# Kernel optimization log

Hardware: AMD Instinct MI355X
Metric: run time of the kernel (lower is better)

The kernel has to match this reference:

```python
import jax, jax.numpy as jnp
import numpy as np
import math

DIM = 1024
NUM_HEADS = 16
SHARED_HEADS = 1
ROUTED_HEADS = 3
HEAD_DIM = DIM // NUM_HEADS
B, N = 2, 2048


def setup_inputs() -> dict:
    key = jax.random.key(0)
    ks = jax.random.split(key, 16)
    s = 1.0 / math.sqrt(DIM)
    inp = {
        "x": jax.random.normal(ks[0], (B, N, DIM), dtype=jnp.float32),
        "Wq": jax.random.uniform(ks[1], (DIM, DIM), minval=-s, maxval=s),
        "bq": jax.random.uniform(ks[2], (DIM,), minval=-s, maxval=s),
        "Wk": jax.random.uniform(ks[3], (DIM, DIM), minval=-s, maxval=s),
        "bk": jax.random.uniform(ks[4], (DIM,), minval=-s, maxval=s),
        "Wv": jax.random.uniform(ks[5], (DIM, DIM), minval=-s, maxval=s),
        "bv": jax.random.uniform(ks[6], (DIM,), minval=-s, maxval=s),
        "Wp": jax.random.uniform(ks[7], (DIM, DIM), minval=-s, maxval=s),
        "bp": jax.random.uniform(ks[8], (DIM,), minval=-s, maxval=s),
        "Wr": jax.random.uniform(ks[9], (NUM_HEADS - SHARED_HEADS, DIM), minval=-s, maxval=s),
        "br": jax.random.uniform(ks[10], (NUM_HEADS - SHARED_HEADS,), minval=-s, maxval=s),
        "Ws": jax.random.uniform(ks[11], (2, DIM), minval=-s, maxval=s),
        "bs": jax.random.uniform(ks[12], (2,), minval=-s, maxval=s),
        # temperature init: log(exp(1/0.24)-1), shape (H,1,1)
        "temperature": jnp.full((NUM_HEADS, 1, 1), float(np.log(np.expm1(1.0 / 0.24))), dtype=jnp.float32),
        "query_embedding": 0.02 * jax.random.normal(ks[13], (NUM_HEADS, 1, HEAD_DIM), dtype=jnp.float32),
    }
    return inp


def reference(x, Wq, bq, Wk, bk, Wv, bv, Wp, bp, Wr, br, Ws, bs, temperature, query_embedding):
    Bsz, Nn, C = x.shape
    H, hd = NUM_HEADS, HEAD_DIM

    def heads(W, b):
        y = x @ W.T + b  # [B,N,C]
        return y.reshape(Bsz, Nn, H, hd).transpose(0, 2, 1, 3)  # [B,H,N,hd]

    q = heads(Wq, bq)
    k = heads(Wk, bk)
    v = heads(Wv, bv)

    q_norm = q / jnp.linalg.norm(q, axis=-1, keepdims=True)
    q_scaled = (q_norm + query_embedding[None]) * jax.nn.softplus(temperature)[None]
    attn = jnp.einsum("bhqd,bhkd->bhqk", q_scaled, k) / math.sqrt(hd)
    attn = jax.nn.softmax(attn, axis=-1)
    h = jnp.einsum("bhqk,bhkd->bhqd", attn, v)
    h = h.transpose(0, 2, 1, 3).reshape(Bsz, Nn, C)  # [B,N,C]

    # routed-head gating
    gates = jax.nn.softmax(h @ Wr.T + br, axis=-1)  # [B,N,H-shared]
    _, idx = jax.lax.top_k(gates, ROUTED_HEADS)
    # NOTE: original uses num_classes=num_heads-shared_heads for one_hot
    mask = jax.nn.one_hot(idx, H - SHARED_HEADS, dtype=gates.dtype).sum(axis=-2)
    routed_gates = gates * mask * ROUTED_HEADS

    sw = jax.nn.softmax(h @ Ws.T + bs, axis=-1)  # [B,N,2]
    shared_gates = sw * SHARED_HEADS
    weight_0 = sw * 2.0
    shared_gates = weight_0[..., 0:1] * shared_gates
    routed_gates = weight_0[..., 1:2] * routed_gates
    masked_gates = jnp.concatenate([shared_gates, routed_gates], axis=-1)

    # einsum('bnc,bnd->bnd') == per-token scalar sum over c times h
    out = h * masked_gates.sum(axis=-1, keepdims=True)
    return out @ Wp.T + bp
```

## Files before the change

### kernel.cpp

```cpp
#include <hip/hip_runtime.h>
#include <hip/hip_bf16.h>

typedef short s16x8 __attribute__((ext_vector_type(8)));
typedef float f32x4 __attribute__((ext_vector_type(4)));
typedef float f32x16 __attribute__((ext_vector_type(16)));

__device__ __forceinline__ float b2f(unsigned short u) {
    union { unsigned int i; float f; } v;
    v.i = ((unsigned int)u) << 16;
    return v.f;
}
__device__ __forceinline__ unsigned int pkbf16(float a, float b) {
    union { __hip_bfloat162 h; unsigned int u; } v;
    v.h = __float22bfloat162_rn(make_float2(a, b));
    return v.u;
}
__device__ __forceinline__ float fast_exp2(float x) {
#if __has_builtin(__builtin_amdgcn_exp2f)
    return __builtin_amdgcn_exp2f(x);
#else
    return exp2f(x);
#endif
}

__device__ __forceinline__ void gl_lds16(const unsigned short* g, unsigned short* l) {
    __builtin_amdgcn_global_load_lds(
        (const __attribute__((address_space(1))) void*)g,
        (__attribute__((address_space(3))) void*)l, 16, 0, 0);
}

__device__ __forceinline__ void perm32swap(unsigned int &a, unsigned int &b) {
    asm("v_permlane32_swap_b32 %0, %1" : "+v"(a), "+v"(b));
}

__device__ __forceinline__ s16x8 mk8(unsigned int a, unsigned int b,
                                     unsigned int c, unsigned int d) {
    union { uint4 u; s16x8 h; } v;
    v.u = make_uint4(a, b, c, d);
    return v.h;
}

__device__ __forceinline__ void cvt8(const float* __restrict__ s,
                                     unsigned short* __restrict__ d, int i) {
    const float* p = s + (size_t)i * 8;
    float4 a = *(const float4*)p;
    float4 b = *(const float4*)(p + 4);
    unsigned int u0 = pkbf16(a.x, a.y), u1 = pkbf16(a.z, a.w);
    unsigned int u2 = pkbf16(b.x, b.y), u3 = pkbf16(b.z, b.w);
    uint4 o = {u0, u1, u2, u3};
    *(uint4*)&d[(size_t)i * 8] = o;
}

__global__ __launch_bounds__(256) void cvt_main(
    const float* __restrict__ x,  const float* __restrict__ Wq,
    const float* __restrict__ Wk, const float* __restrict__ Wv,
    const float* __restrict__ Wr, const float* __restrict__ Ws,
    const float* __restrict__ bq, const float* __restrict__ bk,
    const float* __restrict__ bv,
    unsigned short* __restrict__ xb, unsigned short* __restrict__ wqkv,
    unsigned short* __restrict__ wg, float* __restrict__ bqkv)
{
    int blk = blockIdx.x, t = threadIdx.x;
    if (blk < 2048)      cvt8(x,  xb,             blk * 256 + t);
    else if (blk < 2560) cvt8(Wq, wqkv,           (blk - 2048) * 256 + t);
    else if (blk < 3072) cvt8(Wk, wqkv + 1048576, (blk - 2560) * 256 + t);
    else if (blk < 3584) cvt8(Wv, wqkv + 2097152, (blk - 3072) * 256 + t);
    else if (blk < 3592) { int i = (blk - 3584) * 256 + t; if (i < 1920) cvt8(Wr, wg, i); }
    else if (blk < 3593) { int i = t; cvt8(Ws, wg + 15360, i); }
    else {
        int i = (blk - 3593) * 256 + t;
        bqkv[i] = (i < 1024) ? bq[i] : (i < 2048) ? bk[i - 1024] : bv[i - 2048];
    }
}

__global__ __launch_bounds__(256) void qkv_gemm(
    const unsigned short* __restrict__ A,
    const unsigned short* __restrict__ Bw,
    const float* __restrict__ bias,
    unsigned short* __restrict__ Q, unsigned short* __restrict__ K,
    unsigned short* __restrict__ Vt)
{
    __shared__ __attribute__((aligned(16))) unsigned short As[128 * 64];
    __shared__ __attribute__((aligned(16))) unsigned short Bs[128 * 64];
    const int t = threadIdx.x;
    const int wave = t >> 6, lane = t & 63;
    const int m0 = blockIdx.x * 128, n0 = blockIdx.y * 128;
    const int wm = (wave >> 1) * 64, wn = (wave & 1) * 64;
    const int lr = lane & 15, lq = lane >> 4;
    const int srow = lane >> 3;
    const int scol = (((lane & 7) ^ srow) << 3);

    f32x4 acc[4][4];
#pragma unroll
    for (int i = 0; i < 4; ++i)
#pragma unroll
        for (int j = 0; j < 4; ++j) acc[i][j] = (f32x4){0.f, 0.f, 0.f, 0.f};

    for (int k0 = 0; k0 < 1024; k0 += 64) {
        __syncthreads();
#pragma unroll
        for (int i = 0; i < 4; ++i) {
            int rb = wave * 32 + i * 8;
            gl_lds16(&A[(size_t)(m0 + rb + srow) * 1024 + k0 + scol], &As[rb * 64]);
            gl_lds16(&Bw[(size_t)(n0 + rb + srow) * 1024 + k0 + scol], &Bs[rb * 64]);
        }
        __syncthreads();
#pragma unroll
        for (int kk = 0; kk < 64; kk += 32) {
            const int po = ((((kk >> 3) + lq) ^ (lr & 7)) << 3);
            s16x8 af[4], bf[4];
#pragma unroll
            for (int i = 0; i < 4; ++i)
                af[i] = *(const s16x8*)&As[(wm + i * 16 + lr) * 64 + po];
#pragma unroll
            for (int j = 0; j < 4; ++j)
                bf[j] = *(const s16x8*)&Bs[(wn + j * 16 + lr) * 64 + po];
#pragma unroll
            for (int i = 0; i < 4; ++i)
#pragma unroll
                for (int j = 0; j < 4; ++j)
                    acc[i][j] = __builtin_amdgcn_mfma_f32_16x16x32_bf16(af[i], bf[j], acc[i][j], 0, 0, 0);
        }
    }
    const int kind = n0 >> 10;
    const int nc = n0 & 1023;
    if (kind < 2) {
        unsigned short* Cm = kind ? K : Q;
#pragma unroll
        for (int j = 0; j < 4; ++j) {
            int cl = wn + j * 16 + lr;
            float bv = bias[n0 + cl];
#pragma unroll
            for (int i = 0; i < 4; ++i) {
                int rowb = m0 + wm + i * 16 + lq * 4;
                unsigned int u0 = pkbf16(acc[i][j][0] + bv, acc[i][j][1] + bv);
                unsigned int u1 = pkbf16(acc[i][j][2] + bv, acc[i][j][3] + bv);
                Cm[(size_t)(rowb + 0) * 1024 + nc + cl] = (unsigned short)u0;
                Cm[(size_t)(rowb + 1) * 1024 + nc + cl] = (unsigned short)(u0 >> 16);
                Cm[(size_t)(rowb + 2) * 1024 + nc + cl] = (unsigned short)u1;
                Cm[(size_t)(rowb + 3) * 1024 + nc + cl] = (unsigned short)(u1 >> 16);
            }
        }
    } else {
        const int bb = m0 >> 11;
#pragma unroll
        for (int j = 0; j < 4; ++j) {
            int col = nc + wn + j * 16 + lr;
            int hh = col >> 6, dd = col & 63;
            float bv = bias[n0 + wn + j * 16 + lr];
#pragma unroll
            for (int i = 0; i < 4; ++i) {
                int tokb = m0 + wm + i * 16 + lq * 4;
                int tloc = tokb & 2047;
                uint2 u;
                u.x = pkbf16(acc[i][j][0] + bv, acc[i][j][1] + bv);
                u.y = pkbf16(acc[i][j][2] + bv, acc[i][j][3] + bv);
                *(uint2*)&Vt[((size_t)(bb * 16 + hh) * 64 + dd) * 2048 + tloc] = u;
            }
        }
    }
}

__global__ __launch_bounds__(256) void attn_kernel(
    const unsigned short* __restrict__ Q,
    const unsigned short* __restrict__ Kb,
    const unsigned short* __restrict__ Vt,
    const float* __restrict__ temp,
    const float* __restrict__ qe,
    unsigned short* __restrict__ Hout)
{
    __shared__ __attribute__((aligned(16))) unsigned short Ks[2][64 * 64];
    __shared__ __attribute__((aligned(16))) unsigned short Vs[2][64 * 64];
    __shared__ float Lred[4][32];
    const int t = threadIdx.x, wave = t >> 6, lane = t & 63;
    const int l31 = lane & 31, hi = lane >> 5;
    const int bh = blockIdx.x, b = bh >> 4, h = bh & 15;
    const int q0 = blockIdx.y * 128;
    const int srow = lane >> 3;
    const int scol = (((lane & 7) ^ srow) << 3);
    unsigned short* KsF = &Ks[0][0];

    auto stageK = [&](int kc, int cb) {
#pragma unroll
        for (int i2 = 0; i2 < 2; ++i2) {
            int rb = wave * 16 + i2 * 8;
            gl_lds16(&Kb[(size_t)(b * 2048 + kc + rb + srow) * 1024 + h * 64 + scol],
                     &Ks[cb][rb * 64]);
        }
    };
    auto stageV = [&](int kc, int cb) {
#pragma unroll
        for (int i2 = 0; i2 < 2; ++i2) {
            int rb = wave * 16 + i2 * 8;
            gl_lds16(&Vt[((size_t)(b * 16 + h) * 64 + rb + srow) * 2048 + kc + scol],
                     &Vs[cb][rb * 64]);
        }
    };

#pragma unroll
    for (int i = 0; i < 4; ++i) {
        int rb = wave * 32 + i * 8;
        gl_lds16(&Q[(size_t)(b * 2048 + q0 + rb + srow) * 1024 + h * 64 + scol],
                 &KsF[rb * 64]);
    }
    __syncthreads();

    s16x8 qf[4];
#pragma unroll
    for (int kd = 0; kd < 4; ++kd)
        qf[kd] = *(const s16x8*)&KsF[(wave * 32 + l31) * 64 + (((kd * 2 + hi) ^ (l31 & 7)) << 3)];
    __syncthreads();

    stageK(0, 0);
    stageV(0, 0);

    float tv = temp[h];
    float sp = ((tv > 20.f) ? tv : log1pf(__expf(tv))) * 0.18033688f;
    s16x8 aqB[4];
    {
        float v[4][8];
        float ss = 0.f;
#pragma unroll
        for (int kd = 0; kd < 4; ++kd)
#pragma unroll
            for (int e = 0; e < 8; ++e) {
                v[kd][e] = b2f((unsigned short)qf[kd][e]);
                ss += v[kd][e] * v[kd][e];
            }
        ss += __shfl_xor(ss, 32);
        float rn = rsqrtf(ss);
#pragma unroll
        for (int kd = 0; kd < 4; ++kd) {
            const float* qh = qe + h * 64 + kd * 16 + hi * 8;
            unsigned int w0 = pkbf16((v[kd][0] * rn + qh[0]) * sp, (v[kd][1] * rn + qh[1]) * sp);
            unsigned int w1 = pkbf16((v[kd][2] * rn + qh[2]) * sp, (v[kd][3] * rn + qh[3]) * sp);
            unsigned int w2 = pkbf16((v[kd][4] * rn + qh[4]) * sp, (v[kd][5] * rn + qh[5]) * sp);
            unsigned int w3 = pkbf16((v[kd][6] * rn + qh[6]) * sp, (v[kd][7] * rn + qh[7]) * sp);
            aqB[kd] = mk8(w0, w1, w2, w3);
        }
    }

    f32x16 accO[2];
#pragma unroll
    for (int r = 0; r < 16; ++r) { accO[0][r] = 0.f; accO[1][r] = 0.f; }
    float lsum = 0.f;

    for (int it = 0; it < 32; ++it) {
        const int c = it & 1;
        __syncthreads();
        if (it < 31) { stageK((it + 1) * 64, c ^ 1); stageV((it + 1) * 64, c ^ 1); }

#pragma unroll
        for (int jj = 0; jj < 2; ++jj) {
            const int j = jj ^ (wave & 1);

            s16x8 kf[4];
#pragma unroll
            for (int kd = 0; kd < 4; ++kd)
                kf[kd] = *(const s16x8*)&Ks[c][(j * 32 + l31) * 64 + (((kd * 2 + hi) ^ (l31 & 7)) << 3)];
            f32x16 s;
#pragma unroll
            for (int r = 0; r < 16; ++r) s[r] = 0.f;
            __builtin_amdgcn_s_setprio(1);
#pragma unroll
            for (int kd = 0; kd < 4; ++kd)
                s = __builtin_amdgcn_mfma_f32_32x32x16_bf16(kf[kd], aqB[kd], s, 0, 0, 0);
            __builtin_amdgcn_s_setprio(0);

            float p[16];
#pragma unroll
            for (int r = 0; r < 16; ++r) p[r] = fast_exp2(s[r]);
            lsum += (((p[0] + p[1]) + (p[2] + p[3])) + ((p[4] + p[5]) + (p[6] + p[7])))
                  + (((p[8] + p[9]) + (p[10] + p[11])) + ((p[12] + p[13]) + (p[14] + p[15])));
            unsigned int u[8];
#pragma unroll
            for (int g = 0; g < 8; ++g) u[g] = pkbf16(p[2 * g], p[2 * g + 1]);

#pragma unroll
            for (int kh = 0; kh < 2; ++kh) {
                unsigned int a0 = u[4 * kh + 0], b0 = u[4 * kh + 2];
                unsigned int a1 = u[4 * kh + 1], b1 = u[4 * kh + 3];
                perm32swap(a0, b0);
                perm32swap(a1, b1);
                s16x8 pf = mk8(a0, a1, b0, b1);
                const int vb = (((j * 4 + kh * 2 + hi) ^ (l31 & 7)) << 3);
                s16x8 v0 = *(const s16x8*)&Vs[c][(l31) * 64 + vb];
                s16x8 v1 = *(const s16x8*)&Vs[c][(32 + l31) * 64 + vb];
                __builtin_amdgcn_s_setprio(1);
                accO[0] = __builtin_amdgcn_mfma_f32_32x32x16_bf16(pf, v0, accO[0], 0, 0, 0);
                accO[1] = __builtin_amdgcn_mfma_f32_32x32x16_bf16(pf, v1, accO[1], 0, 0, 0);
                __builtin_amdgcn_s_setprio(0);
            }
        }
    }

    lsum += __shfl_xor(lsum, 32);
    if (hi == 0) Lred[wave][l31] = 1.f / lsum;
    __syncthreads();
    float invv[16];
#pragma unroll
    for (int r = 0; r < 16; ++r)
        invv[r] = Lred[wave][(r & 3) + 8 * (r >> 2) + 4 * hi];
#pragma unroll
    for (int jd = 0; jd < 2; ++jd)
#pragma unroll
        for (int r = 0; r < 16; ++r) {
            int qrow = (r & 3) + 8 * (r >> 2) + 4 * hi;
            float val = accO[jd][r] * invv[r];
            Hout[(size_t)(b * 2048 + q0 + wave * 32 + qrow) * 1024 + h * 64 + jd * 32 + l31] =
                (unsigned short)pkbf16(val, val);
        }
}

__global__ __launch_bounds__(256) void gate_g(
    const unsigned short* __restrict__ Hb,
    const unsigned short* __restrict__ Wg,
    const float* __restrict__ br, const float* __restrict__ bs,
    const float* __restrict__ Wp, unsigned short* __restrict__ wpb,
    float* __restrict__ g)
{
    __shared__ __attribute__((aligned(16))) unsigned short As[4][16 * 64];
    __shared__ __attribute__((aligned(16))) unsigned short Gs[4][32 * 64];
    __shared__ float Lred[4][16][32];
    const int t = threadIdx.x, wave = t >> 6, lane = t & 63;
    const int lr = lane & 15, lq = lane >> 4;
    const int m0 = blockIdx.x * 16;
    const int srow = lane >> 3;
    const int scol = (((lane & 7) ^ srow) << 3);

    cvt8(Wp, wpb, blockIdx.x * 512 + t);
    cvt8(Wp, wpb, blockIdx.x * 512 + 256 + t);

    f32x4 acc[2];
    acc[0] = (f32x4){0.f, 0.f, 0.f, 0.f};
    acc[1] = (f32x4){0.f, 0.f, 0.f, 0.f};

    for (int k0 = wave * 64; k0 < 1024; k0 += 256) {
        gl_lds16(&Hb[(size_t)(m0 + srow) * 1024 + k0 + scol], &As[wave][0]);
        gl_lds16(&Hb[(size_t)(m0 + 8 + srow) * 1024 + k0 + scol], &As[wave][8 * 64]);
#pragma unroll
        for (int i = 0; i < 4; ++i) {
            int row = i * 8 + srow;
            int wr = (row > 16) ? 16 : row;
            gl_lds16(&Wg[(size_t)wr * 1024 + k0 + scol], &Gs[wave][i * 8 * 64]);
        }
        __syncthreads();
#pragma unroll
        for (int kk = 0; kk < 64; kk += 32) {
            const int po = ((((kk >> 3) + lq) ^ (lr & 7)) << 3);
            s16x8 af = *(const s16x8*)&As[wave][lr * 64 + po];
#pragma unroll
            for (int j = 0; j < 2; ++j) {
                s16x8 gf = *(const s16x8*)&Gs[wave][(j * 16 + lr) * 64 + po];
                acc[j] = __builtin_amdgcn_mfma_f32_16x16x32_bf16(af, gf, acc[j], 0, 0, 0);
            }
        }
    }
#pragma unroll
    for (int j = 0; j < 2; ++j)
#pragma unroll
        for (int r = 0; r < 4; ++r)
            Lred[wave][lq * 4 + r][j * 16 + lr] = acc[j][r];
    __syncthreads();
    if (t < 16) {
        float lg[17];
#pragma unroll
        for (int j = 0; j < 17; ++j)
            lg[j] = Lred[0][t][j] + Lred[1][t][j] + Lred[2][t][j] + Lred[3][t][j]
                  + ((j < 15) ? br[j] : bs[j - 15]);
        float mx = lg[0];
#pragma unroll
        for (int j = 1; j < 15; ++j) mx = fmaxf(mx, lg[j]);
        float sum = 0.f, v1 = -1.f, v2 = -1.f, v3 = -1.f;
#pragma unroll
        for (int j = 0; j < 15; ++j) {
            float e = __expf(lg[j] - mx);
            sum += e;
            if (e > v1)      { v3 = v2; v2 = v1; v1 = e; }
            else if (e > v2) { v3 = v2; v2 = e; }
            else if (e > v3) { v3 = e; }
        }
        float tops = (v1 + v2 + v3) / sum;
        float sm = fmaxf(lg[15], lg[16]);
        float e0 = __expf(lg[15] - sm), e1 = __expf(lg[16] - sm);
        float inv = 1.f / (e0 + e1);
        g[m0 + t] = 2.f * (e0 * inv) + 6.f * (e1 * inv) * tops;
    }
}

__global__ __launch_bounds__(256) void gemm64_out(
    const unsigned short* __restrict__ A,
    const unsigned short* __restrict__ Bw,
    const float* __restrict__ bias,
    const float* __restrict__ g,
    float* __restrict__ C)
{
    __shared__ __attribute__((aligned(16))) unsigned short As[64 * 64];
    __shared__ __attribute__((aligned(16))) unsigned short Bs[64 * 64];
    const int t = threadIdx.x, wave = t >> 6, lane = t & 63;
    const int lr = lane & 15, lq = lane >> 4;
    const int m0 = blockIdx.x * 64, n0 = blockIdx.y * 64;
    const int wm = (wave >> 1) * 32, wn = (wave & 1) * 32;
    const int srow = lane >> 3;
    const int scol = (((lane & 7) ^ srow) << 3);

    f32x4 acc[2][2];
#pragma unroll
    for (int i = 0; i < 2; ++i)
#pragma unroll
        for (int j = 0; j < 2; ++j) acc[i][j] = (f32x4){0.f, 0.f, 0.f, 0.f};

    for (int k0 = 0; k0 < 1024; k0 += 64) {
        __syncthreads();
#pragma unroll
        for (int i = 0; i < 2; ++i) {
            int rb = wave * 16 + i * 8;
            gl_lds16(&A[(size_t)(m0 + rb + srow) * 1024 + k0 + scol], &As[rb * 64]);
            gl_lds16(&Bw[(size_t)(n0 + rb + srow) * 1024 + k0 + scol], &Bs[rb * 64]);
        }
        __syncthreads();
#pragma unroll
        for (int kk = 0; kk < 64; kk += 32) {
            const int po = ((((kk >> 3) + lq) ^ (lr & 7)) << 3);
            s16x8 af[2], bf[2];
#pragma unroll
            for (int i = 0; i < 2; ++i)
                af[i] = *(const s16x8*)&As[(wm + i * 16 + lr) * 64 + po];
#pragma unroll
            for (int j = 0; j < 2; ++j)
                bf[j] = *(const s16x8*)&Bs[(wn + j * 16 + lr) * 64 + po];
#pragma unroll
            for (int i = 0; i < 2; ++i)
#pragma unroll
                for (int j = 0; j < 2; ++j)
                    acc[i][j] = __builtin_amdgcn_mfma_f32_16x16x32_bf16(af[i], bf[j], acc[i][j], 0, 0, 0);
        }
    }
#pragma unroll
    for (int i = 0; i < 2; ++i) {
        const float4 gi = *(const float4*)&g[m0 + wm + i * 16 + lq * 4];
        float gv[4] = {gi.x, gi.y, gi.z, gi.w};
#pragma unroll
        for (int j = 0; j < 2; ++j) {
            int col = n0 + wn + j * 16 + lr;
            float bv = bias[col];
            int rowb = m0 + wm + i * 16 + lq * 4;
#pragma unroll
            for (int r = 0; r < 4; ++r)
                C[(size_t)(rowb + r) * 1024 + col] = acc[i][j][r] * gv[r] + bv;
        }
    }
}

extern "C" void kernel_launch(void* const* d_in, const int* in_sizes, int n_in,
                              void* d_out, int out_size, void* d_ws, size_t ws_size,
                              hipStream_t stream)
{
    (void)in_sizes; (void)n_in; (void)out_size; (void)ws_size;
    const float* x   = (const float*)d_in[0];
    const float* Wq  = (const float*)d_in[1];
    const float* bq  = (const float*)d_in[2];
    const float* Wk  = (const float*)d_in[3];
    const float* bk  = (const float*)d_in[4];
    const float* Wv  = (const float*)d_in[5];
    const float* bv  = (const float*)d_in[6];
    const float* Wp  = (const float*)d_in[7];
    const float* bp  = (const float*)d_in[8];
    const float* Wr  = (const float*)d_in[9];
    const float* br  = (const float*)d_in[10];
    const float* Ws  = (const float*)d_in[11];
    const float* bs  = (const float*)d_in[12];
    const float* temperature = (const float*)d_in[13];
    const float* qe  = (const float*)d_in[14];
    float* out = (float*)d_out;

    const size_t MB = 1048576;
    unsigned short* qb   = (unsigned short*)d_ws;
    unsigned short* kb   = (unsigned short*)((char*)d_ws + 8 * MB);
    unsigned short* hb   = (unsigned short*)((char*)d_ws + 16 * MB);
    unsigned short* wqkv = (unsigned short*)((char*)d_ws + 24 * MB);
    unsigned short* wg   = (unsigned short*)((char*)d_ws + 30 * MB);
    float*          bqkv = (float*)((char*)d_ws + 30 * MB + 65536);
    float*          gbuf = (float*)((char*)d_ws + 30 * MB + 131072);
    unsigned short* xb = (unsigned short*)d_out;
    unsigned short* vt = xb + 4 * MB;
    unsigned short* wpb = qb;

    dim3 blk(256);
    cvt_main<<<dim3(3605), blk, 0, stream>>>(x, Wq, Wk, Wv, Wr, Ws, bq, bk, bv,
                                             xb, wqkv, wg, bqkv);
    qkv_gemm<<<dim3(32, 24), blk, 0, stream>>>(xb, wqkv, bqkv, qb, kb, vt);
    attn_kernel<<<dim3(32, 16), blk, 0, stream>>>(qb, kb, vt, temperature, qe, hb);
    gate_g<<<dim3(256), blk, 0, stream>>>(hb, wg, br, bs, Wp, wpb, gbuf);
    gemm64_out<<<dim3(64, 16), blk, 0, stream>>>(hb, wpb, bp, gbuf, out);
}
```

Baseline: 215.8 us.

## Split attention key range across two wave groups per block and merge partials

Attention blocks now run 8 waves: two groups of four each process half of the key sequence for the same 128 queries, using separate double-buffered K/V LDS tiles. After the loop, the second group writes its partial output accumulators to LDS and the first group adds them and divides by the combined row sums. This halves the serial key loop per wave and raises resident waves per CU, at the cost of doubled LDS per block and an extra reduction and barrier at the end.

Measured after the change: 212.5 us. No clear change (-1.5%).

```diff
diff --git a/kernel.cpp b/kernel.cpp
--- a/kernel.cpp
+++ b/kernel.cpp
@@ -161,7 +161,7 @@
     }
 }
 
-__global__ __launch_bounds__(256) void attn_kernel(
+__global__ __launch_bounds__(512, 4) void attn_kernel(
     const unsigned short* __restrict__ Q,
     const unsigned short* __restrict__ Kb,
     const unsigned short* __restrict__ Vt,
@@ -169,46 +169,49 @@
     const float* __restrict__ qe,
     unsigned short* __restrict__ Hout)
 {
-    __shared__ __attribute__((aligned(16))) unsigned short Ks[2][64 * 64];
-    __shared__ __attribute__((aligned(16))) unsigned short Vs[2][64 * 64];
-    __shared__ float Lred[4][32];
+    __shared__ __attribute__((aligned(16))) unsigned short Ks[2][2][64 * 64];
+    __shared__ __attribute__((aligned(16))) unsigned short Vs[2][2][64 * 64];
+    __shared__ float Lred[8][32];
     const int t = threadIdx.x, wave = t >> 6, lane = t & 63;
+    const int ws = wave >> 2, wq = wave & 3;
     const int l31 = lane & 31, hi = lane >> 5;
     const int bh = blockIdx.x, b = bh >> 4, h = bh & 15;
     const int q0 = blockIdx.y * 128;
     const int srow = lane >> 3;
     const int scol = (((lane & 7) ^ srow) << 3);
-    unsigned short* KsF = &Ks[0][0];
+    const int kbase = ws << 10;
+    unsigned short* KsF = &Ks[0][0][0];
 
     auto stageK = [&](int kc, int cb) {
 #pragma unroll
         for (int i2 = 0; i2 < 2; ++i2) {
-            int rb = wave * 16 + i2 * 8;
-            gl_lds16(&Kb[(size_t)(b * 2048 + kc + rb + srow) * 1024 + h * 64 + scol],
-                     &Ks[cb][rb * 64]);
+            int rb = wq * 16 + i2 * 8;
+            gl_lds16(&Kb[(size_t)(b * 2048 + kbase + kc + rb + srow) * 1024 + h * 64 + scol],
+                     &Ks[ws][cb][rb * 64]);
         }
     };
     auto stageV = [&](int kc, int cb) {
 #pragma unroll
         for (int i2 = 0; i2 < 2; ++i2) {
-            int rb = wave * 16 + i2 * 8;
-            gl_lds16(&Vt[((size_t)(b * 16 + h) * 64 + rb + srow) * 2048 + kc + scol],
-                     &Vs[cb][rb * 64]);
+            int rb = wq * 16 + i2 * 8;
+            gl_lds16(&Vt[((size_t)(b * 16 + h) * 64 + rb + srow) * 2048 + kbase + kc + scol],
+                     &Vs[ws][cb][rb * 64]);
         }
     };
 
-#pragma unroll
-    for (int i = 0; i < 4; ++i) {
-        int rb = wave * 32 + i * 8;
+    {
+        int rb = wave * 16;
         gl_lds16(&Q[(size_t)(b * 2048 + q0 + rb + srow) * 1024 + h * 64 + scol],
                  &KsF[rb * 64]);
+        gl_lds16(&Q[(size_t)(b * 2048 + q0 + rb + 8 + srow) * 1024 + h * 64 + scol],
+                 &KsF[(rb + 8) * 64]);
     }
     __syncthreads();
 
     s16x8 qf[4];
 #pragma unroll
     for (int kd = 0; kd < 4; ++kd)
-        qf[kd] = *(const s16x8*)&KsF[(wave * 32 + l31) * 64 + (((kd * 2 + hi) ^ (l31 & 7)) << 3)];
+        qf[kd] = *(const s16x8*)&KsF[(wq * 32 + l31) * 64 + (((kd * 2 + hi) ^ (l31 & 7)) << 3)];
     __syncthreads();
 
     stageK(0, 0);
@@ -245,10 +248,10 @@
     for (int r = 0; r < 16; ++r) { accO[0][r] = 0.f; accO[1][r] = 0.f; }
     float lsum = 0.f;
 
-    for (int it = 0; it < 32; ++it) {
+    for (int it = 0; it < 16; ++it) {
         const int c = it & 1;
         __syncthreads();
-        if (it < 31) { stageK((it + 1) * 64, c ^ 1); stageV((it + 1) * 64, c ^ 1); }
+        if (it < 15) { stageK((it + 1) * 64, c ^ 1); stageV((it + 1) * 64, c ^ 1); }
 
 #pragma unroll
         for (int jj = 0; jj < 2; ++jj) {
@@ -257,7 +260,7 @@
             s16x8 kf[4];
 #pragma unroll
             for (int kd = 0; kd < 4; ++kd)
-                kf[kd] = *(const s16x8*)&Ks[c][(j * 32 + l31) * 64 + (((kd * 2 + hi) ^ (l31 & 7)) << 3)];
+                kf[kd] = *(const s16x8*)&Ks[ws][c][(j * 32 + l31) * 64 + (((kd * 2 + hi) ^ (l31 & 7)) << 3)];
             f32x16 s;
 #pragma unroll
             for (int r = 0; r < 16; ++r) s[r] = 0.f;
@@ -284,8 +287,8 @@
                 perm32swap(a1, b1);
                 s16x8 pf = mk8(a0, a1, b0, b1);
                 const int vb = (((j * 4 + kh * 2 + hi) ^ (l31 & 7)) << 3);
-                s16x8 v0 = *(const s16x8*)&Vs[c][(l31) * 64 + vb];
-                s16x8 v1 = *(const s16x8*)&Vs[c][(32 + l31) * 64 + vb];
+                s16x8 v0 = *(const s16x8*)&Vs[ws][c][(l31) * 64 + vb];
+                s16x8 v1 = *(const s16x8*)&Vs[ws][c][(32 + l31) * 64 + vb];
                 __builtin_amdgcn_s_setprio(1);
                 accO[0] = __builtin_amdgcn_mfma_f32_32x32x16_bf16(pf, v0, accO[0], 0, 0, 0);
                 accO[1] = __builtin_amdgcn_mfma_f32_32x32x16_bf16(pf, v1, accO[1], 0, 0, 0);
@@ -295,21 +298,43 @@
     }
 
     lsum += __shfl_xor(lsum, 32);
-    if (hi == 0) Lred[wave][l31] = 1.f / lsum;
+    if (hi == 0) Lred[wave][l31] = lsum;
     __syncthreads();
-    float invv[16];
-#pragma unroll
-    for (int r = 0; r < 16; ++r)
-        invv[r] = Lred[wave][(r & 3) + 8 * (r >> 2) + 4 * hi];
-#pragma unroll
-    for (int jd = 0; jd < 2; ++jd)
-#pragma unroll
-        for (int r = 0; r < 16; ++r) {
-            int qrow = (r & 3) + 8 * (r >> 2) + 4 * hi;
-            float val = accO[jd][r] * invv[r];
-            Hout[(size_t)(b * 2048 + q0 + wave * 32 + qrow) * 1024 + h * 64 + jd * 32 + l31] =
-                (unsigned short)pkbf16(val, val);
-        }
+
+    float* mb = (wq < 2) ? (float*)&Ks[0][wq][0] : (float*)&Vs[0][wq - 2][0];
+    if (ws == 1) {
+#pragma unroll
+        for (int jd = 0; jd < 2; ++jd)
+#pragma unroll
+            for (int rg = 0; rg < 4; ++rg) {
+                f32x4 vv = { accO[jd][rg * 4 + 0], accO[jd][rg * 4 + 1],
+                             accO[jd][rg * 4 + 2], accO[jd][rg * 4 + 3] };
+                *(f32x4*)&mb[((jd * 4 + rg) << 8) + (lane << 2)] = vv;
+            }
+    }
+    __syncthreads();
+    if (ws == 0) {
+#pragma unroll
+        for (int jd = 0; jd < 2; ++jd)
+#pragma unroll
+            for (int rg = 0; rg < 4; ++rg) {
+                f32x4 vv = *(const f32x4*)&mb[((jd * 4 + rg) << 8) + (lane << 2)];
+                accO[jd][rg * 4 + 0] += vv[0];
+                accO[jd][rg * 4 + 1] += vv[1];
+                accO[jd][rg * 4 + 2] += vv[2];
+                accO[jd][rg * 4 + 3] += vv[3];
+            }
+#pragma unroll
+        for (int jd = 0; jd < 2; ++jd)
+#pragma unroll
+            for (int r = 0; r < 16; ++r) {
+                int qrow = (r & 3) + 8 * (r >> 2) + 4 * hi;
+                float inv = 1.f / (Lred[wq][qrow] + Lred[wq + 4][qrow]);
+                float val = accO[jd][r] * inv;
+                Hout[(size_t)(b * 2048 + q0 + wq * 32 + qrow) * 1024 + h * 64 + jd * 32 + l31] =
+                    (unsigned short)pkbf16(val, val);
+            }
+    }
 }
 
 __global__ __launch_bounds__(256) void gate_g(
@@ -490,7 +515,7 @@
     cvt_main<<<dim3(3605), blk, 0, stream>>>(x, Wq, Wk, Wv, Wr, Ws, bq, bk, bv,
                                              xb, wqkv, wg, bqkv);
     qkv_gemm<<<dim3(32, 24), blk, 0, stream>>>(xb, wqkv, bqkv, qb, kb, vt);
-    attn_kernel<<<dim3(32, 16), blk, 0, stream>>>(qb, kb, vt, temperature, qe, hb);
+    attn_kernel<<<dim3(32, 16), dim3(512), 0, stream>>>(qb, kb, vt, temperature, qe, hb);
     gate_g<<<dim3(256), blk, 0, stream>>>(hb, wg, br, bs, Wp, wpb, gbuf);
     gemm64_out<<<dim3(64, 16), blk, 0, stream>>>(hb, wpb, bp, gbuf, out);
 }
```
